# Performance work log

Hardware: AMD Instinct MI355X
Metric: run time of the kernel (lower is better)

Reference implementation:

```python
import jax, jax.numpy as jnp
import numpy as np
from jax import lax

D = 1024  # inputSize == hidden size
B = 128   # batch
T = 256   # step


def setup_inputs() -> dict:
    key = jax.random.key(0)
    ks = jax.random.split(key, 9)
    s = 1.0 / np.sqrt(D)  # torch LSTMCell/Linear default init scale
    return {
        "inp": jax.random.normal(ks[0], (B, T, D), dtype=jnp.float32),
        "h0": jnp.zeros((B, D), dtype=jnp.float32),
        "c0": jnp.zeros((B, D), dtype=jnp.float32),
        "W_ih": jax.random.uniform(ks[1], (4 * D, D), jnp.float32, -s, s),
        "W_hh": jax.random.uniform(ks[2], (4 * D, D), jnp.float32, -s, s),
        "b_ih": jax.random.uniform(ks[3], (4 * D,), jnp.float32, -s, s),
        "b_hh": jax.random.uniform(ks[4], (4 * D,), jnp.float32, -s, s),
        "fc_w": jax.random.uniform(ks[5], (1, D), jnp.float32, -s, s),
        "fc_b": jax.random.uniform(ks[6], (1,), jnp.float32, -s, s),
        "step": T,
    }


def reference(inp, h0, c0, W_ih, W_hh, b_ih, b_hh, fc_w, fc_b, step):
    # The original's double python loop just transposes [B, T, D] -> [T, B, D].
    xs = jnp.swapaxes(inp, 0, 1)  # [T, B, D]

    def cell(carry, x):
        h, c = carry
        # torch.nn.LSTMCell gate order: i, f, g, o
        gates = x @ W_ih.T + b_ih + h @ W_hh.T + b_hh  # [B, 4D]
        i, f, g, o = jnp.split(gates, 4, axis=-1)
        i = jax.nn.sigmoid(i)
        f = jax.nn.sigmoid(f)
        g = jnp.tanh(g)
        o = jax.nn.sigmoid(o)
        c2 = f * c + i * g
        h2 = o * jnp.tanh(c2)
        return (h2, c2), None

    (hx, cx), _ = lax.scan(cell, (h0, c0), xs)
    yhat = jax.nn.sigmoid(hx @ fc_w.T + fc_b)  # [B, 1]
    return (yhat, hx, cx)
```

## Files before the change

kernel.cpp:

```cpp
#include <hip/hip_runtime.h>
#include <hip/hip_cooperative_groups.h>

namespace cg = cooperative_groups;

#define Dd 1024
#define Bb 128
#define Tt 256
#define NWG 256
#define NTHR 256

typedef short bf16x8 __attribute__((ext_vector_type(8)));
typedef float f32x4 __attribute__((ext_vector_type(4)));
typedef unsigned int u32x4 __attribute__((ext_vector_type(4)));
typedef unsigned long long u64;

static __device__ __forceinline__ unsigned short f2bf(float x) {
  unsigned int u = __float_as_uint(x);
  u += 0x7fffu + ((u >> 16) & 1u);
  return (unsigned short)(u >> 16);
}
static __device__ __forceinline__ unsigned int pk2(float a, float b) {
  return (unsigned int)f2bf(a) | ((unsigned int)f2bf(b) << 16);
}
static __device__ __forceinline__ bf16x8 as_bf(uint4 u) {
  union { uint4 u; bf16x8 v; } x; x.u = u; return x.v;
}
static __device__ __forceinline__ f32x4 mfma_(bf16x8 a, bf16x8 b, f32x4 c) {
  return __builtin_amdgcn_mfma_f32_16x16x32_bf16(a, b, c, 0, 0, 0);
}
static __device__ __forceinline__ float sigm(float x) { return 1.f / (1.f + __expf(-x)); }
static __device__ __forceinline__ float tanh_s(float x) { return 1.f - 2.f / (__expf(2.f * x) + 1.f); }
static __device__ __forceinline__ u64 aload(const u64* p) {
  return __hip_atomic_load(p, __ATOMIC_RELAXED, __HIP_MEMORY_SCOPE_AGENT);
}

template<int RING>
__global__ void __launch_bounds__(NTHR, 1) lstm_kernel(
    const float* __restrict__ inp, const float* __restrict__ h0,
    const float* __restrict__ c0, const float* __restrict__ W_ih,
    const float* __restrict__ W_hh, const float* __restrict__ b_ih,
    const float* __restrict__ b_hh, const float* __restrict__ fc_w,
    const float* __restrict__ fc_b, float* __restrict__ out,
    int* __restrict__ flags, unsigned short* __restrict__ hbuf,
    unsigned short* __restrict__ xbf, int use_xbf)
{
  extern __shared__ uint4 ldsW[];
  __shared__ float red[4];
  __shared__ int sent;

  const int tid = threadIdx.x;
  const int wg  = blockIdx.x;
  const int gid = wg * NTHR + tid;
  cg::grid_group grid = cg::this_grid();

  const int gs = wg >> 1;
  const int bh = wg & 1;

  if (tid < 4)
    __hip_atomic_store(&flags[bh * 512 + gs * 4 + tid], 0,
                       __ATOMIC_RELAXED, __HIP_MEMORY_SCOPE_AGENT);
  if (tid == 0) sent = -1;

  if (use_xbf) {
    for (int i = gid; i < Tt * Bb * (Dd / 8); i += NWG * NTHR) {
      int d8 = i & 127, b = (i >> 7) & 127, t = i >> 14;
      const float* s = inp + ((size_t)b * Tt + t) * Dd + d8 * 8;
      uint4 p;
      p.x = pk2(s[0], s[1]); p.y = pk2(s[2], s[3]);
      p.z = pk2(s[4], s[5]); p.w = pk2(s[6], s[7]);
      *(uint4*)(xbf + (size_t)i * 8) = p;
    }
  }
  uint4* hb4w = (uint4*)hbuf;
  for (int i = gid; i < 128 * 128; i += NWG * NTHR) {
    int row = i & 127, gsl = i >> 7;
    const float* s = h0 + (size_t)row * Dd + gsl * 8;
    uint4 p;
    p.x = pk2(s[0], s[1]); p.y = pk2(s[2], s[3]);
    p.z = pk2(s[4], s[5]); p.w = pk2(s[6], s[7]);
    hb4w[gsl * 128 + row] = p;
  }

  for (int i = tid; i < 8192; i += NTHR) {
    int l2 = i & 63, mmct = (i >> 6) & 3, kc = i >> 8;
    int cc = l2 & 15, ct = mmct & 1;
    int row = (((ct << 1) | (cc >> 3)) << 10) | (gs << 3) | (cc & 7);
    int k = kc * 32 + ((l2 >> 4) << 3);
    const float* s = ((mmct & 2) ? W_hh : W_ih) + (size_t)row * Dd + k;
    uint4 p;
    p.x = pk2(s[0], s[1]); p.y = pk2(s[2], s[3]);
    p.z = pk2(s[4], s[5]); p.w = pk2(s[6], s[7]);
    ldsW[i] = p;
  }

  const int w = tid >> 6, l = tid & 63;
  const int c = l & 15;
  const int rowbase = bh * 64 + w * 16;
  const int arow = rowbase + c;
  const int koff8 = l >> 4;
  const int r0 = ((c >> 3) << 10) | (gs << 3) | (c & 7);
  const int r1 = ((2 + (c >> 3)) << 10) | (gs << 3) | (c & 7);
  const float bias0 = b_ih[r0] + b_hh[r0];
  const float bias1 = b_ih[r1] + b_hh[r1];
  const int dim = (gs << 3) | (c & 7);
  const int crow = rowbase + (koff8 << 2);
  float creg[4];
  #pragma unroll
  for (int j = 0; j < 4; ++j) creg[j] = c0[(size_t)(crow + j) * Dd + dim];

  float* out_y = out;
  float* out_h = out + Bb;
  float* out_c = out + Bb + (size_t)Bb * Dd;

  int* myflag = &flags[bh * 512 + gs * 4 + w];
  const u64* fq = (const u64*)(flags + bh * 512);
  const int shbase = ((l & 15) >> 2) * 16;

  grid.sync();

  for (int t = 0; t < Tt; ++t) {
    const int rslot = RING ? t : (t & 1);
    const int wslot = RING ? (t + 1) : ((t + 1) & 1);

    f32x4 xa0 = {bias0, bias0, bias0, bias0};
    f32x4 xa1 = {bias1, bias1, bias1, bias1};
    f32x4 xb0 = {0.f, 0.f, 0.f, 0.f};
    f32x4 xb1 = {0.f, 0.f, 0.f, 0.f};

    if (use_xbf) {
      const uint4* xA = (const uint4*)(xbf + ((size_t)t * Bb + arow) * Dd + koff8 * 8);
      #pragma unroll
      for (int kc = 0; kc < 32; kc += 2) {
        uint4 ax0 = xA[kc * 4];
        uint4 ax1 = xA[(kc + 1) * 4];
        const int lb0 = kc * 256 + l, lb1 = (kc + 1) * 256 + l;
        xa0 = mfma_(as_bf(ax0), as_bf(ldsW[lb0]),      xa0);
        xa1 = mfma_(as_bf(ax0), as_bf(ldsW[lb0 + 64]), xa1);
        xb0 = mfma_(as_bf(ax1), as_bf(ldsW[lb1]),      xb0);
        xb1 = mfma_(as_bf(ax1), as_bf(ldsW[lb1 + 64]), xb1);
      }
    } else {
      const float* xF = inp + ((size_t)arow * Tt + t) * Dd + koff8 * 8;
      #pragma unroll 4
      for (int kc = 0; kc < 32; ++kc) {
        const float* xs = xF + kc * 32;
        uint4 axu;
        axu.x = pk2(xs[0], xs[1]); axu.y = pk2(xs[2], xs[3]);
        axu.z = pk2(xs[4], xs[5]); axu.w = pk2(xs[6], xs[7]);
        const int lb = kc * 256 + l;
        xa0 = mfma_(as_bf(axu), as_bf(ldsW[lb]),      xa0);
        xa1 = mfma_(as_bf(axu), as_bf(ldsW[lb + 64]), xa1);
      }
    }

    if (w == 0) {
      int ok;
      do {
        u64 a = aload(&fq[l]);
        u64 b = aload(&fq[l + 64]);
        u64 c2 = aload(&fq[l + 128]);
        u64 d2 = aload(&fq[l + 192]);
        ok = ((int)a >= t) && ((int)(a >> 32) >= t) &&
             ((int)b >= t) && ((int)(b >> 32) >= t) &&
             ((int)c2 >= t) && ((int)(c2 >> 32) >= t) &&
             ((int)d2 >= t) && ((int)(d2 >> 32) >= t);
      } while (!__all(ok));
      __hip_atomic_store(&sent, t, __ATOMIC_RELEASE, __HIP_MEMORY_SCOPE_WORKGROUP);
    } else {
      while (__hip_atomic_load(&sent, __ATOMIC_ACQUIRE, __HIP_MEMORY_SCOPE_WORKGROUP) < t) {}
    }
    asm volatile("" ::: "memory");

    if constexpr (RING) {
      const uint4* hA4 = (const uint4*)(hbuf + (size_t)rslot * 131072);
      #pragma unroll
      for (int kc = 0; kc < 32; kc += 2) {
        uint4 h0u = hA4[(kc * 4 + koff8) * 128 + arow];
        uint4 h1u = hA4[((kc + 1) * 4 + koff8) * 128 + arow];
        const int lb0 = kc * 256 + l, lb1 = (kc + 1) * 256 + l;
        xa0 = mfma_(as_bf(h0u), as_bf(ldsW[lb0 + 128]), xa0);
        xa1 = mfma_(as_bf(h0u), as_bf(ldsW[lb0 + 192]), xa1);
        xb0 = mfma_(as_bf(h1u), as_bf(ldsW[lb1 + 128]), xb0);
        xb1 = mfma_(as_bf(h1u), as_bf(ldsW[lb1 + 192]), xb1);
      }
    } else {
      const u64* hA = (const u64*)hbuf + (size_t)rslot * 32768;
      #pragma unroll
      for (int kc = 0; kc < 32; kc += 2) {
        const int hi0 = (kc * 4 + koff8) * 256 + arow * 2;
        const int hi1 = ((kc + 1) * 4 + koff8) * 256 + arow * 2;
        union { u64 q[2]; uint4 p4; } h0u, h1u;
        h0u.q[0] = aload(&hA[hi0]); h0u.q[1] = aload(&hA[hi0 + 1]);
        h1u.q[0] = aload(&hA[hi1]); h1u.q[1] = aload(&hA[hi1 + 1]);
        const int lb0 = kc * 256 + l, lb1 = (kc + 1) * 256 + l;
        xa0 = mfma_(as_bf(h0u.p4), as_bf(ldsW[lb0 + 128]), xa0);
        xa1 = mfma_(as_bf(h0u.p4), as_bf(ldsW[lb0 + 192]), xa1);
        xb0 = mfma_(as_bf(h1u.p4), as_bf(ldsW[lb1 + 128]), xb0);
        xb1 = mfma_(as_bf(h1u.p4), as_bf(ldsW[lb1 + 192]), xb1);
      }
    }
    f32x4 acc0 = xa0 + xb0;
    f32x4 acc1 = xa1 + xb1;

    float fo0[4], fo1[4];
    #pragma unroll
    for (int j = 0; j < 4; ++j) {
      fo0[j] = __shfl_xor(acc0[j], 8);
      fo1[j] = __shfl_xor(acc1[j], 8);
    }
    unsigned int bfu0 = 0, bfu1 = 0, bfu2 = 0, bfu3 = 0;
    if (c < 8) {
      float hnv[4];
      #pragma unroll
      for (int j = 0; j < 4; ++j) {
        float iv = sigm(acc0[j]);
        float fv = sigm(fo0[j]);
        float gv = tanh_s(acc1[j]);
        float ov = sigm(fo1[j]);
        float cn = fv * creg[j] + iv * gv;
        float hn = ov * tanh_s(cn);
        creg[j] = cn;
        hnv[j] = hn;
        if (t == Tt - 1) {
          size_t off = (size_t)(crow + j) * Dd + dim;
          __hip_atomic_store(&out_h[off], hn, __ATOMIC_RELAXED, __HIP_MEMORY_SCOPE_AGENT);
          __hip_atomic_store(&out_c[off], cn, __ATOMIC_RELAXED, __HIP_MEMORY_SCOPE_AGENT);
        }
      }
      bfu0 = f2bf(hnv[0]); bfu1 = f2bf(hnv[1]);
      bfu2 = f2bf(hnv[2]); bfu3 = f2bf(hnv[3]);
    }

    unsigned int w0 = 0, w1 = 0, w2 = 0, w3 = 0;
    #pragma unroll
    for (int j = 0; j < 4; ++j) {
      unsigned int src = (j == 0) ? bfu0 : (j == 1) ? bfu1 : (j == 2) ? bfu2 : bfu3;
      unsigned int lo0 = __shfl((int)src, shbase + 0);
      unsigned int hi0g = __shfl((int)src, shbase + 1);
      unsigned int lo1 = __shfl((int)src, shbase + 2);
      unsigned int hi1g = __shfl((int)src, shbase + 3);
      unsigned int lo2 = __shfl((int)src, shbase + 4);
      unsigned int hi2g = __shfl((int)src, shbase + 5);
      unsigned int lo3 = __shfl((int)src, shbase + 6);
      unsigned int hi3g = __shfl((int)src, shbase + 7);
      bool mine = ((l & 3) == j);
      if (mine) {
        w0 = lo0 | (hi0g << 16);
        w1 = lo1 | (hi1g << 16);
        w2 = lo2 | (hi2g << 16);
        w3 = lo3 | (hi3g << 16);
      }
    }
    if (l < 16) {
      u32x4 val = {w0, w1, w2, w3};
      unsigned short* hw = hbuf + (size_t)wslot * 131072
                           + (size_t)gs * 1024 + (size_t)(rowbase + l) * 8;
      asm volatile("global_store_dwordx4 %0, %1, off sc0 sc1"
                   :: "v"(hw), "v"(val) : "memory");
    }
    asm volatile("s_waitcnt vmcnt(0)" ::: "memory");
    if (l == 0)
      __hip_atomic_store(myflag, t + 1, __ATOMIC_RELAXED, __HIP_MEMORY_SCOPE_AGENT);
  }

  if (wg < Bb) {
    {
      const u64* fa = (const u64*)flags;
      int ok;
      do {
        ok = 1;
        #pragma unroll
        for (int r = 0; r < 8; ++r) {
          u64 v = aload(&fa[l + r * 64]);
          ok &= ((int)v >= Tt) && ((int)(v >> 32) >= Tt);
        }
      } while (!__all(ok));
    }
    const u64* hr = (const u64*)(out_h + (size_t)wg * Dd);
    float s = 0.f;
    for (int k = tid; k < Dd / 2; k += NTHR) {
      u64 v = aload(&hr[k]);
      union { u64 u; float f[2]; } q; q.u = v;
      s += q.f[0] * fc_w[2 * k] + q.f[1] * fc_w[2 * k + 1];
    }
    #pragma unroll
    for (int off = 32; off > 0; off >>= 1) s += __shfl_down(s, off);
    if (l == 0) red[w] = s;
    __syncthreads();
    if (tid == 0) {
      float tot = red[0] + red[1] + red[2] + red[3] + fc_b[0];
      out_y[wg] = sigm(tot);
    }
  }
}

extern "C" void kernel_launch(void* const* d_in, const int* in_sizes, int n_in,
                              void* d_out, int out_size, void* d_ws, size_t ws_size,
                              hipStream_t stream) {
  (void)in_sizes; (void)n_in; (void)out_size;
  const float* inp  = (const float*)d_in[0];
  const float* h0   = (const float*)d_in[1];
  const float* c0   = (const float*)d_in[2];
  const float* W_ih = (const float*)d_in[3];
  const float* W_hh = (const float*)d_in[4];
  const float* b_ih = (const float*)d_in[5];
  const float* b_hh = (const float*)d_in[6];
  const float* fc_w = (const float*)d_in[7];
  const float* fc_b = (const float*)d_in[8];
  float* out = (float*)d_out;

  const size_t fbytes = 4096;
  const size_t slot   = (size_t)Bb * Dd * 2;
  const size_t ring1  = (size_t)(Tt + 1) * slot;
  const size_t ring0  = 2 * slot;
  const size_t xbytes = (size_t)Tt * Bb * Dd * 2;

  int ring, use_xbf;
  size_t rbytes;
  if (ws_size >= fbytes + ring1 + xbytes)      { ring = 1; use_xbf = 1; rbytes = ring1; }
  else if (ws_size >= fbytes + ring1)          { ring = 1; use_xbf = 0; rbytes = ring1; }
  else if (ws_size >= fbytes + ring0 + xbytes) { ring = 0; use_xbf = 1; rbytes = ring0; }
  else                                         { ring = 0; use_xbf = 0; rbytes = ring0; }

  int* flags = (int*)d_ws;
  unsigned short* hbuf = (unsigned short*)((char*)d_ws + fbytes);
  unsigned short* xbf  = (unsigned short*)((char*)d_ws + fbytes + rbytes);

  void* kfn = ring ? (void*)lstm_kernel<1> : (void*)lstm_kernel<0>;
  (void)hipFuncSetAttribute((const void*)kfn,
                            hipFuncAttributeMaxDynamicSharedMemorySize, 131072);

  void* kargs[] = {(void*)&inp, (void*)&h0, (void*)&c0, (void*)&W_ih, (void*)&W_hh,
                   (void*)&b_ih, (void*)&b_hh, (void*)&fc_w, (void*)&fc_b,
                   (void*)&out, (void*)&flags, (void*)&hbuf, (void*)&xbf, (void*)&use_xbf};
  (void)hipLaunchCooperativeKernel(kfn, dim3(NWG), dim3(NTHR),
                                   kargs, 131072u, stream);
}
```

Measured before the change: 2.878 ms.

## Replace per-wave flag polling with per-step sharded atomic counters

Each wave now does an atomic fetch-add on a per-timestep counter, sharded by wave index and batch half, instead of storing its own flag. Every wave polls just four counters for the current step, where before wave 0 scanned 512 flags and relayed the result through LDS. This cuts the polling traffic and drops the intra-workgroup handoff from the critical path of every timestep. In exchange, 128 workgroups contend with atomics on the same few counter addresses each step, and all four waves in a workgroup now spin on global memory.

```diff
diff --git a/kernel.cpp b/kernel.cpp
--- a/kernel.cpp
+++ b/kernel.cpp
@@ -41,12 +41,11 @@
     const float* __restrict__ W_hh, const float* __restrict__ b_ih,
     const float* __restrict__ b_hh, const float* __restrict__ fc_w,
     const float* __restrict__ fc_b, float* __restrict__ out,
-    int* __restrict__ flags, unsigned short* __restrict__ hbuf,
+    int* __restrict__ cnt, unsigned short* __restrict__ hbuf,
     unsigned short* __restrict__ xbf, int use_xbf)
 {
   extern __shared__ uint4 ldsW[];
   __shared__ float red[4];
-  __shared__ int sent;
 
   const int tid = threadIdx.x;
   const int wg  = blockIdx.x;
@@ -56,10 +55,10 @@
   const int gs = wg >> 1;
   const int bh = wg & 1;
 
-  if (tid < 4)
-    __hip_atomic_store(&flags[bh * 512 + gs * 4 + tid], 0,
-                       __ATOMIC_RELAXED, __HIP_MEMORY_SCOPE_AGENT);
-  if (tid == 0) sent = -1;
+  for (int i = gid; i < 2 * 257 * 4; i += NWG * NTHR) {
+    int t = (i >> 2) % 257;
+    cnt[i] = (t == 0) ? 128 : 0;
+  }
 
   if (use_xbf) {
     for (int i = gid; i < Tt * Bb * (Dd / 8); i += NWG * NTHR) {
@@ -112,8 +111,9 @@
   float* out_h = out + Bb;
   float* out_c = out + Bb + (size_t)Bb * Dd;
 
-  int* myflag = &flags[bh * 512 + gs * 4 + w];
-  const u64* fq = (const u64*)(flags + bh * 512);
+  int* myshard_base = cnt + bh * 257 * 4 + w;
+  const int cbase = bh * 257 * 4;
+
   const int shbase = ((l & 15) >> 2) * 16;
 
   grid.sync();
@@ -153,21 +153,15 @@
       }
     }
 
-    if (w == 0) {
-      int ok;
+    {
+      const u64* cq = (const u64*)(cnt + cbase + t * 4);
+      int okf;
       do {
-        u64 a = aload(&fq[l]);
-        u64 b = aload(&fq[l + 64]);
-        u64 c2 = aload(&fq[l + 128]);
-        u64 d2 = aload(&fq[l + 192]);
-        ok = ((int)a >= t) && ((int)(a >> 32) >= t) &&
-             ((int)b >= t) && ((int)(b >> 32) >= t) &&
-             ((int)c2 >= t) && ((int)(c2 >> 32) >= t) &&
-             ((int)d2 >= t) && ((int)(d2 >> 32) >= t);
-      } while (!__all(ok));
-      __hip_atomic_store(&sent, t, __ATOMIC_RELEASE, __HIP_MEMORY_SCOPE_WORKGROUP);
-    } else {
-      while (__hip_atomic_load(&sent, __ATOMIC_ACQUIRE, __HIP_MEMORY_SCOPE_WORKGROUP) < t) {}
+        u64 a = aload(&cq[0]);
+        u64 b = aload(&cq[1]);
+        okf = ((int)a >= 128) && ((int)(a >> 32) >= 128) &&
+              ((int)b >= 128) && ((int)(b >> 32) >= 128);
+      } while (!okf);
     }
     asm volatile("" ::: "memory");
 
@@ -260,21 +254,25 @@
     }
     asm volatile("s_waitcnt vmcnt(0)" ::: "memory");
     if (l == 0)
-      __hip_atomic_store(myflag, t + 1, __ATOMIC_RELAXED, __HIP_MEMORY_SCOPE_AGENT);
+      __hip_atomic_fetch_add(myshard_base + (t + 1) * 4, 1,
+                             __ATOMIC_RELAXED, __HIP_MEMORY_SCOPE_AGENT);
   }
 
   if (wg < Bb) {
     {
-      const u64* fa = (const u64*)flags;
-      int ok;
+      const u64* c0q = (const u64*)(cnt + 0 * 257 * 4 + Tt * 4);
+      const u64* c1q = (const u64*)(cnt + 1 * 257 * 4 + Tt * 4);
+      int okf;
       do {
-        ok = 1;
-        #pragma unroll
-        for (int r = 0; r < 8; ++r) {
-          u64 v = aload(&fa[l + r * 64]);
-          ok &= ((int)v >= Tt) && ((int)(v >> 32) >= Tt);
-        }
-      } while (!__all(ok));
+        u64 a = aload(&c0q[0]);
+        u64 b = aload(&c0q[1]);
+        u64 e = aload(&c1q[0]);
+        u64 f = aload(&c1q[1]);
+        okf = ((int)a >= 128) && ((int)(a >> 32) >= 128) &&
+              ((int)b >= 128) && ((int)(b >> 32) >= 128) &&
+              ((int)e >= 128) && ((int)(e >> 32) >= 128) &&
+              ((int)f >= 128) && ((int)(f >> 32) >= 128);
+      } while (!okf);
     }
     const u64* hr = (const u64*)(out_h + (size_t)wg * Dd);
     float s = 0.f;
@@ -309,7 +307,7 @@
   const float* fc_b = (const float*)d_in[8];
   float* out = (float*)d_out;
 
-  const size_t fbytes = 4096;
+  const size_t fbytes = 16384;
   const size_t slot   = (size_t)Bb * Dd * 2;
   const size_t ring1  = (size_t)(Tt + 1) * slot;
   const size_t ring0  = 2 * slot;
@@ -322,7 +320,7 @@
   else if (ws_size >= fbytes + ring0 + xbytes) { ring = 0; use_xbf = 1; rbytes = ring0; }
   else                                         { ring = 0; use_xbf = 0; rbytes = ring0; }
 
-  int* flags = (int*)d_ws;
+  int* cnt = (int*)d_ws;
   unsigned short* hbuf = (unsigned short*)((char*)d_ws + fbytes);
   unsigned short* xbf  = (unsigned short*)((char*)d_ws + fbytes + rbytes);
 
@@ -332,7 +330,7 @@
 
   void* kargs[] = {(void*)&inp, (void*)&h0, (void*)&c0, (void*)&W_ih, (void*)&W_hh,
                    (void*)&b_ih, (void*)&b_hh, (void*)&fc_w, (void*)&fc_b,
-                   (void*)&out, (void*)&flags, (void*)&hbuf, (void*)&xbf, (void*)&use_xbf};
+                   (void*)&out, (void*)&cnt, (void*)&hbuf, (void*)&xbf, (void*)&use_xbf};
   (void)hipLaunchCooperativeKernel(kfn, dim3(NWG), dim3(NTHR),
                                    kargs, 131072u, stream);
 }
```

Result: slower. 4.040 ms (+40.4%).

## Split per-step h readiness wait into four K-quarter flag groups

Applied to the files above, without the earlier changes.

Reorders the per-step flag layout so each quarter of the hidden-state K dimension maps to its own contiguous block of producer flags. In the ring path, the consumer now waits only for the producers of the current K quarter before running that quarter's MFMAs, so the recurrent matmul can overlap with stragglers still publishing later quarters. It also adds s_sleep backoff in the polling loops and has only one wave poll at the end before a workgroup barrier. The trade-off is four wait/handoff rounds per step instead of one, plus possible extra latency from the sleep.

```diff
diff --git a/kernel.cpp b/kernel.cpp
--- a/kernel.cpp
+++ b/kernel.cpp
@@ -46,7 +46,7 @@
 {
   extern __shared__ uint4 ldsW[];
   __shared__ float red[4];
-  __shared__ int sent;
+  __shared__ int sentq[4];
 
   const int tid = threadIdx.x;
   const int wg  = blockIdx.x;
@@ -57,9 +57,9 @@
   const int bh = wg & 1;
 
   if (tid < 4)
-    __hip_atomic_store(&flags[bh * 512 + gs * 4 + tid], 0,
-                       __ATOMIC_RELAXED, __HIP_MEMORY_SCOPE_AGENT);
-  if (tid == 0) sent = -1;
+    __hip_atomic_store(&flags[bh * 512 + (gs >> 5) * 128 + ((gs & 31) << 2) + tid],
+                       0, __ATOMIC_RELAXED, __HIP_MEMORY_SCOPE_AGENT);
+  if (tid < 4) sentq[tid] = -1;
 
   if (use_xbf) {
     for (int i = gid; i < Tt * Bb * (Dd / 8); i += NWG * NTHR) {
@@ -112,8 +112,7 @@
   float* out_h = out + Bb;
   float* out_c = out + Bb + (size_t)Bb * Dd;
 
-  int* myflag = &flags[bh * 512 + gs * 4 + w];
-  const u64* fq = (const u64*)(flags + bh * 512);
+  int* myflag = &flags[bh * 512 + (gs >> 5) * 128 + ((gs & 31) << 2) + w];
   const int shbase = ((l & 15) >> 2) * 16;
 
   grid.sync();
@@ -153,37 +152,57 @@
       }
     }
 
-    if (w == 0) {
-      int ok;
-      do {
-        u64 a = aload(&fq[l]);
-        u64 b = aload(&fq[l + 64]);
-        u64 c2 = aload(&fq[l + 128]);
-        u64 d2 = aload(&fq[l + 192]);
-        ok = ((int)a >= t) && ((int)(a >> 32) >= t) &&
-             ((int)b >= t) && ((int)(b >> 32) >= t) &&
-             ((int)c2 >= t) && ((int)(c2 >> 32) >= t) &&
-             ((int)d2 >= t) && ((int)(d2 >> 32) >= t);
-      } while (!__all(ok));
-      __hip_atomic_store(&sent, t, __ATOMIC_RELEASE, __HIP_MEMORY_SCOPE_WORKGROUP);
-    } else {
-      while (__hip_atomic_load(&sent, __ATOMIC_ACQUIRE, __HIP_MEMORY_SCOPE_WORKGROUP) < t) {}
-    }
-    asm volatile("" ::: "memory");
-
     if constexpr (RING) {
       const uint4* hA4 = (const uint4*)(hbuf + (size_t)rslot * 131072);
       #pragma unroll
-      for (int kc = 0; kc < 32; kc += 2) {
-        uint4 h0u = hA4[(kc * 4 + koff8) * 128 + arow];
-        uint4 h1u = hA4[((kc + 1) * 4 + koff8) * 128 + arow];
-        const int lb0 = kc * 256 + l, lb1 = (kc + 1) * 256 + l;
-        xa0 = mfma_(as_bf(h0u), as_bf(ldsW[lb0 + 128]), xa0);
-        xa1 = mfma_(as_bf(h0u), as_bf(ldsW[lb0 + 192]), xa1);
-        xb0 = mfma_(as_bf(h1u), as_bf(ldsW[lb1 + 128]), xb0);
-        xb1 = mfma_(as_bf(h1u), as_bf(ldsW[lb1 + 192]), xb1);
+      for (int q = 0; q < 4; ++q) {
+        if (w == 0) {
+          const u64* fqq = (const u64*)(flags + bh * 512 + q * 128);
+          u64 v = aload(&fqq[l]);
+          int ok = ((int)v >= t) && ((int)(v >> 32) >= t);
+          while (!__all(ok)) {
+            __builtin_amdgcn_s_sleep(1);
+            v = aload(&fqq[l]);
+            ok = ((int)v >= t) && ((int)(v >> 32) >= t);
+          }
+          if (l == 0)
+            __hip_atomic_store(&sentq[q], t, __ATOMIC_RELEASE, __HIP_MEMORY_SCOPE_WORKGROUP);
+        } else {
+          while (__hip_atomic_load(&sentq[q], __ATOMIC_ACQUIRE, __HIP_MEMORY_SCOPE_WORKGROUP) < t) {}
+        }
+        asm volatile("" ::: "memory");
+        #pragma unroll
+        for (int kp = 0; kp < 4; ++kp) {
+          const int kc = q * 8 + kp * 2;
+          uint4 h0u = hA4[(kc * 4 + koff8) * 128 + arow];
+          uint4 h1u = hA4[((kc + 1) * 4 + koff8) * 128 + arow];
+          const int lb0 = kc * 256 + l, lb1 = (kc + 1) * 256 + l;
+          xa0 = mfma_(as_bf(h0u), as_bf(ldsW[lb0 + 128]), xa0);
+          xa1 = mfma_(as_bf(h0u), as_bf(ldsW[lb0 + 192]), xa1);
+          xb0 = mfma_(as_bf(h1u), as_bf(ldsW[lb1 + 128]), xb0);
+          xb1 = mfma_(as_bf(h1u), as_bf(ldsW[lb1 + 192]), xb1);
+        }
       }
     } else {
+      if (w == 0) {
+        const u64* fq = (const u64*)(flags + bh * 512);
+        int ok;
+        do {
+          u64 a = aload(&fq[l]);
+          u64 b = aload(&fq[l + 64]);
+          u64 c2 = aload(&fq[l + 128]);
+          u64 d2 = aload(&fq[l + 192]);
+          ok = ((int)a >= t) && ((int)(a >> 32) >= t) &&
+               ((int)b >= t) && ((int)(b >> 32) >= t) &&
+               ((int)c2 >= t) && ((int)(c2 >> 32) >= t) &&
+               ((int)d2 >= t) && ((int)(d2 >> 32) >= t);
+        } while (!__all(ok));
+        if (l == 0)
+          __hip_atomic_store(&sentq[0], t, __ATOMIC_RELEASE, __HIP_MEMORY_SCOPE_WORKGROUP);
+      } else {
+        while (__hip_atomic_load(&sentq[0], __ATOMIC_ACQUIRE, __HIP_MEMORY_SCOPE_WORKGROUP) < t) {}
+      }
+      asm volatile("" ::: "memory");
       const u64* hA = (const u64*)hbuf + (size_t)rslot * 32768;
       #pragma unroll
       for (int kc = 0; kc < 32; kc += 2) {
@@ -264,7 +283,7 @@
   }
 
   if (wg < Bb) {
-    {
+    if (w == 0) {
       const u64* fa = (const u64*)flags;
       int ok;
       do {
@@ -274,8 +293,10 @@
           u64 v = aload(&fa[l + r * 64]);
           ok &= ((int)v >= Tt) && ((int)(v >> 32) >= Tt);
         }
+        if (!__all(ok)) { __builtin_amdgcn_s_sleep(1); ok = 0; }
       } while (!__all(ok));
     }
+    __syncthreads();
     const u64* hr = (const u64*)(out_h + (size_t)wg * Dd);
     float s = 0.f;
     for (int k = tid; k < Dd / 2; k += NTHR) {
@@ -309,7 +330,7 @@
   const float* fc_b = (const float*)d_in[8];
   float* out = (float*)d_out;
 
-  const size_t fbytes = 4096;
+  const size_t fbytes = 16384;
   const size_t slot   = (size_t)Bb * Dd * 2;
   const size_t ring1  = (size_t)(Tt + 1) * slot;
   const size_t ring0  = 2 * slot;
```

Measured after the change: 3.963 ms. 37.7% more time.

## Precompute next-step input projection after h store; batch-prefetch h loads

Applied to the files above, without the earlier changes.

Moves the input-projection MFMA work for step t+1 to the end of step t, after the new h slice is stored and before the completion flag is published, so accumulators arrive pre-seeded. The ring-path h loads are restructured into groups of eight register-prefetched loads to overlap global latency with MFMAs. The intent is to overlap x-projection work with cross-workgroup h propagation. Because the vmcnt(0) wait now also covers the x loads, flag publication may be delayed, which puts the x GEMM on the critical path of the recurrence. The flag region is also enlarged.

```diff
diff --git a/kernel.cpp b/kernel.cpp
--- a/kernel.cpp
+++ b/kernel.cpp
@@ -118,29 +118,27 @@
 
   grid.sync();
 
-  for (int t = 0; t < Tt; ++t) {
-    const int rslot = RING ? t : (t & 1);
-    const int wslot = RING ? (t + 1) : ((t + 1) & 1);
-
-    f32x4 xa0 = {bias0, bias0, bias0, bias0};
-    f32x4 xa1 = {bias1, bias1, bias1, bias1};
-    f32x4 xb0 = {0.f, 0.f, 0.f, 0.f};
-    f32x4 xb1 = {0.f, 0.f, 0.f, 0.f};
-
+  f32x4 pa0, pa1, pb0, pb1;
+
+  {
+    pa0 = f32x4{bias0, bias0, bias0, bias0};
+    pa1 = f32x4{bias1, bias1, bias1, bias1};
+    pb0 = f32x4{0.f, 0.f, 0.f, 0.f};
+    pb1 = f32x4{0.f, 0.f, 0.f, 0.f};
     if (use_xbf) {
-      const uint4* xA = (const uint4*)(xbf + ((size_t)t * Bb + arow) * Dd + koff8 * 8);
+      const uint4* xA = (const uint4*)(xbf + ((size_t)0 * Bb + arow) * Dd + koff8 * 8);
       #pragma unroll
       for (int kc = 0; kc < 32; kc += 2) {
         uint4 ax0 = xA[kc * 4];
         uint4 ax1 = xA[(kc + 1) * 4];
         const int lb0 = kc * 256 + l, lb1 = (kc + 1) * 256 + l;
-        xa0 = mfma_(as_bf(ax0), as_bf(ldsW[lb0]),      xa0);
-        xa1 = mfma_(as_bf(ax0), as_bf(ldsW[lb0 + 64]), xa1);
-        xb0 = mfma_(as_bf(ax1), as_bf(ldsW[lb1]),      xb0);
-        xb1 = mfma_(as_bf(ax1), as_bf(ldsW[lb1 + 64]), xb1);
+        pa0 = mfma_(as_bf(ax0), as_bf(ldsW[lb0]),      pa0);
+        pa1 = mfma_(as_bf(ax0), as_bf(ldsW[lb0 + 64]), pa1);
+        pb0 = mfma_(as_bf(ax1), as_bf(ldsW[lb1]),      pb0);
+        pb1 = mfma_(as_bf(ax1), as_bf(ldsW[lb1 + 64]), pb1);
       }
     } else {
-      const float* xF = inp + ((size_t)arow * Tt + t) * Dd + koff8 * 8;
+      const float* xF = inp + ((size_t)arow * Tt + 0) * Dd + koff8 * 8;
       #pragma unroll 4
       for (int kc = 0; kc < 32; ++kc) {
         const float* xs = xF + kc * 32;
@@ -148,10 +146,15 @@
         axu.x = pk2(xs[0], xs[1]); axu.y = pk2(xs[2], xs[3]);
         axu.z = pk2(xs[4], xs[5]); axu.w = pk2(xs[6], xs[7]);
         const int lb = kc * 256 + l;
-        xa0 = mfma_(as_bf(axu), as_bf(ldsW[lb]),      xa0);
-        xa1 = mfma_(as_bf(axu), as_bf(ldsW[lb + 64]), xa1);
-      }
-    }
+        pa0 = mfma_(as_bf(axu), as_bf(ldsW[lb]),      pa0);
+        pa1 = mfma_(as_bf(axu), as_bf(ldsW[lb + 64]), pa1);
+      }
+    }
+  }
+
+  for (int t = 0; t < Tt; ++t) {
+    const int rslot = RING ? t : (t & 1);
+    const int wslot = RING ? (t + 1) : ((t + 1) & 1);
 
     if (w == 0) {
       int ok;
@@ -173,15 +176,29 @@
 
     if constexpr (RING) {
       const uint4* hA4 = (const uint4*)(hbuf + (size_t)rslot * 131072);
-      #pragma unroll
-      for (int kc = 0; kc < 32; kc += 2) {
-        uint4 h0u = hA4[(kc * 4 + koff8) * 128 + arow];
-        uint4 h1u = hA4[((kc + 1) * 4 + koff8) * 128 + arow];
-        const int lb0 = kc * 256 + l, lb1 = (kc + 1) * 256 + l;
-        xa0 = mfma_(as_bf(h0u), as_bf(ldsW[lb0 + 128]), xa0);
-        xa1 = mfma_(as_bf(h0u), as_bf(ldsW[lb0 + 192]), xa1);
-        xb0 = mfma_(as_bf(h1u), as_bf(ldsW[lb1 + 128]), xb0);
-        xb1 = mfma_(as_bf(h1u), as_bf(ldsW[lb1 + 192]), xb1);
+      uint4 hc[8], hn[8];
+      #pragma unroll
+      for (int i = 0; i < 8; ++i) hc[i] = hA4[(i * 4 + koff8) * 128 + arow];
+      #pragma unroll
+      for (int oct = 0; oct < 4; ++oct) {
+        if (oct < 3) {
+          #pragma unroll
+          for (int i = 0; i < 8; ++i)
+            hn[i] = hA4[(((oct + 1) * 8 + i) * 4 + koff8) * 128 + arow];
+        }
+        #pragma unroll
+        for (int i = 0; i < 8; i += 2) {
+          const int kc = oct * 8 + i;
+          const int lb0 = kc * 256 + l, lb1 = (kc + 1) * 256 + l;
+          pa0 = mfma_(as_bf(hc[i]),     as_bf(ldsW[lb0 + 128]), pa0);
+          pa1 = mfma_(as_bf(hc[i]),     as_bf(ldsW[lb0 + 192]), pa1);
+          pb0 = mfma_(as_bf(hc[i + 1]), as_bf(ldsW[lb1 + 128]), pb0);
+          pb1 = mfma_(as_bf(hc[i + 1]), as_bf(ldsW[lb1 + 192]), pb1);
+        }
+        if (oct < 3) {
+          #pragma unroll
+          for (int i = 0; i < 8; ++i) hc[i] = hn[i];
+        }
       }
     } else {
       const u64* hA = (const u64*)hbuf + (size_t)rslot * 32768;
@@ -193,14 +210,14 @@
         h0u.q[0] = aload(&hA[hi0]); h0u.q[1] = aload(&hA[hi0 + 1]);
         h1u.q[0] = aload(&hA[hi1]); h1u.q[1] = aload(&hA[hi1 + 1]);
         const int lb0 = kc * 256 + l, lb1 = (kc + 1) * 256 + l;
-        xa0 = mfma_(as_bf(h0u.p4), as_bf(ldsW[lb0 + 128]), xa0);
-        xa1 = mfma_(as_bf(h0u.p4), as_bf(ldsW[lb0 + 192]), xa1);
-        xb0 = mfma_(as_bf(h1u.p4), as_bf(ldsW[lb1 + 128]), xb0);
-        xb1 = mfma_(as_bf(h1u.p4), as_bf(ldsW[lb1 + 192]), xb1);
-      }
-    }
-    f32x4 acc0 = xa0 + xb0;
-    f32x4 acc1 = xa1 + xb1;
+        pa0 = mfma_(as_bf(h0u.p4), as_bf(ldsW[lb0 + 128]), pa0);
+        pa1 = mfma_(as_bf(h0u.p4), as_bf(ldsW[lb0 + 192]), pa1);
+        pb0 = mfma_(as_bf(h1u.p4), as_bf(ldsW[lb1 + 128]), pb0);
+        pb1 = mfma_(as_bf(h1u.p4), as_bf(ldsW[lb1 + 192]), pb1);
+      }
+    }
+    f32x4 acc0 = pa0 + pb0;
+    f32x4 acc1 = pa1 + pb1;
 
     float fo0[4], fo1[4];
     #pragma unroll
@@ -218,12 +235,12 @@
         float gv = tanh_s(acc1[j]);
         float ov = sigm(fo1[j]);
         float cn = fv * creg[j] + iv * gv;
-        float hn = ov * tanh_s(cn);
+        float hn2 = ov * tanh_s(cn);
         creg[j] = cn;
-        hnv[j] = hn;
+        hnv[j] = hn2;
         if (t == Tt - 1) {
           size_t off = (size_t)(crow + j) * Dd + dim;
-          __hip_atomic_store(&out_h[off], hn, __ATOMIC_RELAXED, __HIP_MEMORY_SCOPE_AGENT);
+          __hip_atomic_store(&out_h[off], hn2, __ATOMIC_RELAXED, __HIP_MEMORY_SCOPE_AGENT);
           __hip_atomic_store(&out_c[off], cn, __ATOMIC_RELAXED, __HIP_MEMORY_SCOPE_AGENT);
         }
       }
@@ -258,6 +275,39 @@
       asm volatile("global_store_dwordx4 %0, %1, off sc0 sc1"
                    :: "v"(hw), "v"(val) : "memory");
     }
+
+    pa0 = f32x4{bias0, bias0, bias0, bias0};
+    pa1 = f32x4{bias1, bias1, bias1, bias1};
+    pb0 = f32x4{0.f, 0.f, 0.f, 0.f};
+    pb1 = f32x4{0.f, 0.f, 0.f, 0.f};
+    if (t < Tt - 1) {
+      if (use_xbf) {
+        const uint4* xA = (const uint4*)(xbf + ((size_t)(t + 1) * Bb + arow) * Dd + koff8 * 8);
+        #pragma unroll
+        for (int kc = 0; kc < 32; kc += 2) {
+          uint4 ax0 = xA[kc * 4];
+          uint4 ax1 = xA[(kc + 1) * 4];
+          const int lb0 = kc * 256 + l, lb1 = (kc + 1) * 256 + l;
+          pa0 = mfma_(as_bf(ax0), as_bf(ldsW[lb0]),      pa0);
+          pa1 = mfma_(as_bf(ax0), as_bf(ldsW[lb0 + 64]), pa1);
+          pb0 = mfma_(as_bf(ax1), as_bf(ldsW[lb1]),      pb0);
+          pb1 = mfma_(as_bf(ax1), as_bf(ldsW[lb1 + 64]), pb1);
+        }
+      } else {
+        const float* xF = inp + ((size_t)arow * Tt + (t + 1)) * Dd + koff8 * 8;
+        #pragma unroll 4
+        for (int kc = 0; kc < 32; ++kc) {
+          const float* xs = xF + kc * 32;
+          uint4 axu;
+          axu.x = pk2(xs[0], xs[1]); axu.y = pk2(xs[2], xs[3]);
+          axu.z = pk2(xs[4], xs[5]); axu.w = pk2(xs[6], xs[7]);
+          const int lb = kc * 256 + l;
+          pa0 = mfma_(as_bf(axu), as_bf(ldsW[lb]),      pa0);
+          pa1 = mfma_(as_bf(axu), as_bf(ldsW[lb + 64]), pa1);
+        }
+      }
+    }
+
     asm volatile("s_waitcnt vmcnt(0)" ::: "memory");
     if (l == 0)
       __hip_atomic_store(myflag, t + 1, __ATOMIC_RELAXED, __HIP_MEMORY_SCOPE_AGENT);
@@ -309,7 +359,7 @@
   const float* fc_b = (const float*)d_in[8];
   float* out = (float*)d_out;
 
-  const size_t fbytes = 4096;
+  const size_t fbytes = 16384;
   const size_t slot   = (size_t)Bb * Dd * 2;
   const size_t ring1  = (size_t)(Tt + 1) * slot;
   const size_t ring0  = 2 * slot;
```

Result: no change. 2.914 ms (+1.3%).
